# Optimization experiments

Hardware: AMD Instinct MI355X
Metric: run time of the kernel (lower is better)

The kernel has to match this reference:

```python
import jax, jax.numpy as jnp
import numpy as np

N_ITERS = 3   # Routing default n_iters
EPS = 1e-5    # variance floor added to sig2
LN_EPS = 1e-5 # torch LayerNorm eps


def _routing(a_inp, mu_inp, W, Bias, beta_use, beta_ign):
    """Heinsen routing (gaussian p_model).
    a_inp: [b, n_i]; mu_inp: [b, n_i, c, d_inp]
    W: [1 or n_i, n_o, d_inp, d_out]; Bias: [n_o, c, d_out]; betas: [n_o].
    """
    if W.shape[0] == 1:  # weights shared across input capsules (n_inp not fixed)
        V = jnp.einsum('jdh,bicd->bijch', W[0], mu_inp) + Bias
    else:
        V = jnp.einsum('ijdh,bicd->bijch', W, mu_inp) + Bias
    n_out = V.shape[2]
    fa = jax.nn.sigmoid(a_inp)[..., None]          # [b, n_i, 1]
    R = jnp.full(V.shape[:3], 1.0 / n_out, dtype=V.dtype)
    a_out = mu_out = sig2 = Vm2 = None
    for it in range(N_ITERS):
        # E-step
        if it > 0:
            log_p = (-jnp.einsum('bijch,bjch->bij', Vm2, 1.0 / (2.0 * sig2))
                     - 0.5 * jnp.log(sig2).sum(axis=(-2, -1))[:, None, :])
            R = jax.nn.softmax(jax.nn.log_sigmoid(a_out)[:, None, :] + log_p, axis=-1)
        # D-step
        D_use = fa * R                              # [b, n_i, n_o]
        D_sum = D_use.sum(axis=-2)                  # [b, n_o]
        # M-step
        a_out = beta_use * D_sum - beta_ign * (fa.sum(axis=-2) - D_sum)
        nR = D_use / D_sum[:, None, :]
        mu_out = jnp.einsum('bij,bijch->bjch', nR, V)
        Vm2 = jnp.square(V - mu_out[:, None])
        sig2 = jnp.einsum('bij,bijch->bjch', nR, Vm2) + EPS
    return a_out, mu_out, sig2


def setup_inputs() -> dict:
    B, T = 32, 128
    d_depth, d_emb, d_cap, n_parts, n_classes = 13, 1024, 16, 64, 5
    key = jax.random.key(0)
    ks = jax.random.split(key, 8)
    mask = jax.random.uniform(ks[0], (B, T), jnp.float32, 0.05, 0.95)  # in (0,1) so logit is finite
    embs = jax.random.normal(ks[1], (B, T, d_depth, d_emb), jnp.float32)
    depth_emb = jax.random.normal(ks[2], (d_depth, d_emb), jnp.float32) * 0.02
    ln_w = jnp.ones((d_emb,), jnp.float32)
    ln_b = jnp.zeros((d_emb,), jnp.float32)
    dp_w = jax.random.normal(ks[3], (n_parts, d_emb), jnp.float32) * np.sqrt(2.0 / d_emb)  # kaiming
    dp_b = jnp.zeros((n_parts,), jnp.float32)
    # Routing 1: d_cov=1, d_inp=n_parts, d_out=d_cap, n_out=n_parts, n_inp shared (-1)
    W1 = jax.random.normal(ks[4], (1, n_parts, n_parts, d_cap), jnp.float32) / n_parts
    B1 = jnp.zeros((n_parts, 1, d_cap), jnp.float32)
    bu1 = jnp.zeros((n_parts,), jnp.float32)
    bi1 = jnp.zeros((n_parts,), jnp.float32)
    # Routing 2: d_cov=1, d_inp=d_cap, d_out=d_cap, n_out=n_classes, n_inp=n_parts
    W2 = jax.random.normal(ks[5], (n_parts, n_classes, d_cap, d_cap), jnp.float32) / d_cap
    B2 = jnp.zeros((n_classes, 1, d_cap), jnp.float32)
    bu2 = jnp.zeros((n_classes,), jnp.float32)
    bi2 = jnp.zeros((n_classes,), jnp.float32)
    return dict(mask=mask, embs=embs, depth_emb=depth_emb, ln_w=ln_w, ln_b=ln_b,
                dp_w=dp_w, dp_b=dp_b, W1=W1, B1=B1, bu1=bu1, bi1=bi1,
                W2=W2, B2=B2, bu2=bu2, bi2=bi2)


def reference(mask, embs, depth_emb, ln_w, ln_b, dp_w, dp_b,
              W1, B1, bu1, bi1, W2, B2, bu2, bi2):
    B = mask.shape[0]
    d_depth = embs.shape[-2]
    # input activations: logit(mask), repeated over depth
    a = jnp.log(mask / (1.0 - mask))                       # [B, T]
    a = jnp.broadcast_to(a[..., None], a.shape + (d_depth,)).reshape(B, -1)  # [B, T*d_depth]
    # detect_parts: LayerNorm -> Linear -> Swish
    x = embs + depth_emb
    m = x.mean(axis=-1, keepdims=True)
    v = ((x - m) ** 2).mean(axis=-1, keepdims=True)        # biased var (torch LayerNorm)
    xn = (x - m) * jax.lax.rsqrt(v + LN_EPS) * ln_w + ln_b
    h = jnp.einsum('btde,pe->btdp', xn, dp_w) + dp_b
    mu = h * jax.nn.sigmoid(h)                             # Swish
    mu = mu.reshape(B, -1, 1, mu.shape[-1])                # [B, T*d_depth, 1, n_parts]
    a, mu, sig2 = _routing(a, mu, W1, B1, bu1, bi1)
    a, mu, sig2 = _routing(a, mu, W2, B2, bu2, bi2)
    return a, mu, sig2
```

## Files before the change

kernel.cpp:

```cpp
#include <hip/hip_runtime.h>
#include <hip/hip_bf16.h>

constexpr int BQ = 32;
constexpr int TT = 128;
constexpr int DD = 13;
constexpr int E  = 1024;
constexpr int P  = 64;
constexpr int C  = 16;
constexpr int NC = 5;
constexpr int NI = TT * DD;
constexpr int NROWS = BQ * NI;
constexpr int S1 = 1092;

__global__ void k_sumfa(const float* __restrict__ mask, float* __restrict__ sumfa)
{
    const int b = blockIdx.x, tid = threadIdx.x;
    float v = mask[b * TT + tid];
#pragma unroll
    for (int off = 32; off > 0; off >>= 1) v += __shfl_xor(v, off);
    __shared__ float p2[2];
    if ((tid & 63) == 0) p2[tid >> 6] = v;
    __syncthreads();
    if (tid == 0) sumfa[b] = (float)DD * (p2[0] + p2[1]);
}

__global__ void k0_pre(const float* __restrict__ ln_w, const float* __restrict__ ln_b,
                       const float* __restrict__ dp_w, const float* __restrict__ dp_b,
                       const float* __restrict__ W1,
                       float* __restrict__ c1t, float* __restrict__ c2t,
                       float* __restrict__ W1m)
{
    const int blk = blockIdx.x, tid = threadIdx.x;
    if (blk < 64) {
        float a0 = 0.f, a1 = 0.f;
        for (int k = tid; k < E; k += 256) {
            const float wv = dp_w[(size_t)blk * E + k];
            a0 = fmaf(ln_w[k], wv, a0);
            a1 = fmaf(ln_b[k], wv, a1);
        }
#pragma unroll
        for (int off = 32; off > 0; off >>= 1) {
            a0 += __shfl_xor(a0, off);
            a1 += __shfl_xor(a1, off);
        }
        __shared__ float r2[2][4];
        if ((tid & 63) == 0) { r2[0][tid >> 6] = a0; r2[1][tid >> 6] = a1; }
        __syncthreads();
        if (tid == 0) {
            c1t[blk] = r2[0][0] + r2[0][1] + r2[0][2] + r2[0][3];
            c2t[blk] = r2[1][0] + r2[1][1] + r2[1][2] + r2[1][3] + dp_b[blk];
        }
    } else {
        const int t = (blk - 64) * 256 + tid;
        const int d = t >> 10, col = t & 1023;
        W1m[t] = W1[((size_t)(col >> 4) * 64 + d) * 16 + (col & 15)];
    }
}

__global__ __launch_bounds__(256, 2) void
k1a(const float* __restrict__ embs, const float* __restrict__ depth_emb,
    const float* __restrict__ ln_w, const float* __restrict__ dp_w,
    const float* __restrict__ c1t, const float* __restrict__ c2t,
    float* __restrict__ V)
{
    __shared__ float xs[16 * S1];
    __shared__ float rmean[16], rrstd[16];
    float* hpar = xs;
    const int tid = threadIdx.x;
    const int c4 = tid & 15, q = tid >> 4;
    const int wv = tid >> 6;
    const int row0 = blockIdx.x * 64;

    for (int rt = 0; rt < 4; ++rt) {
        const int r0g = row0 + rt * 16;
        {
            const int sr = tid >> 4;
            const int sk = (tid & 15) * 4;
            const int grow = r0g + sr;
            const float* xr = embs + (size_t)grow * E;
            const float* dr = depth_emb + (size_t)(grow % DD) * E;
            float s = 0.f, s2 = 0.f;
#pragma unroll
            for (int m = 0; m < 16; ++m) {
                const int k = sk + m * 64;
                float4 a = *reinterpret_cast<const float4*>(xr + k);
                const float4 dd = *reinterpret_cast<const float4*>(dr + k);
                a.x += dd.x; a.y += dd.y; a.z += dd.z; a.w += dd.w;
                *reinterpret_cast<float4*>(xs + sr * S1 + sk + m * 68) = a;
                s += a.x + a.y + a.z + a.w;
                s2 = fmaf(a.x, a.x, fmaf(a.y, a.y, fmaf(a.z, a.z, fmaf(a.w, a.w, s2))));
            }
#pragma unroll
            for (int off = 8; off > 0; off >>= 1) {
                s += __shfl_xor(s, off);
                s2 += __shfl_xor(s2, off);
            }
            if ((tid & 15) == 0) {
                const float mean = s * (1.f / E);
                const float var = s2 * (1.f / E) - mean * mean;
                rmean[sr] = mean;
                rrstd[sr] = rsqrtf(var + 1e-5f);
            }
        }
        __syncthreads();
        float acc[16][4];
#pragma unroll
        for (int r = 0; r < 16; ++r)
#pragma unroll
            for (int cc = 0; cc < 4; ++cc) acc[r][cc] = 0.f;

        for (int sub = 0; sub < 4; ++sub) {
            const int kb = q * 64 + sub * 16;
            float4 wr_[4][4];
            {
                float4 lw[4];
#pragma unroll
                for (int f = 0; f < 4; ++f)
                    lw[f] = *reinterpret_cast<const float4*>(ln_w + kb + f * 4);
#pragma unroll
                for (int cc = 0; cc < 4; ++cc) {
                    const float* wp = dp_w + (size_t)(c4 * 4 + cc) * E + kb;
#pragma unroll
                    for (int f = 0; f < 4; ++f) {
                        float4 t = *reinterpret_cast<const float4*>(wp + f * 4);
                        t.x *= lw[f].x; t.y *= lw[f].y; t.z *= lw[f].z; t.w *= lw[f].w;
                        wr_[cc][f] = t;
                    }
                }
            }
            const int xbase = q * 68 + sub * 16;
#pragma unroll
            for (int r = 0; r < 16; ++r) {
#pragma unroll
                for (int f = 0; f < 4; ++f) {
                    const float4 x4 = *reinterpret_cast<const float4*>(xs + r * S1 + xbase + f * 4);
#pragma unroll
                    for (int cc = 0; cc < 4; ++cc) {
                        acc[r][cc] = fmaf(x4.x, wr_[cc][f].x, acc[r][cc]);
                        acc[r][cc] = fmaf(x4.y, wr_[cc][f].y, acc[r][cc]);
                        acc[r][cc] = fmaf(x4.z, wr_[cc][f].z, acc[r][cc]);
                        acc[r][cc] = fmaf(x4.w, wr_[cc][f].w, acc[r][cc]);
                    }
                }
            }
        }
#pragma unroll
        for (int r = 0; r < 16; ++r)
#pragma unroll
            for (int cc = 0; cc < 4; ++cc) {
                float v = acc[r][cc];
                v += __shfl_xor(v, 16);
                v += __shfl_xor(v, 32);
                acc[r][cc] = v;
            }
        __syncthreads();
        if ((tid & 48) == 0) {
#pragma unroll
            for (int r = 0; r < 16; ++r)
                *reinterpret_cast<float4*>(hpar + ((wv * 16 + r) * 68 + c4 * 4)) =
                    make_float4(acc[r][0], acc[r][1], acc[r][2], acc[r][3]);
        }
        __syncthreads();
        {
            const int er = tid >> 4, ec = tid & 15;
            float4 sum = make_float4(0.f, 0.f, 0.f, 0.f);
#pragma unroll
            for (int w = 0; w < 4; ++w) {
                const float4 hp = *reinterpret_cast<const float4*>(hpar + ((w * 16 + er) * 68 + ec * 4));
                sum.x += hp.x; sum.y += hp.y; sum.z += hp.z; sum.w += hp.w;
            }
            const float mean = rmean[er], rstd = rrstd[er];
            const float4 cv1 = *reinterpret_cast<const float4*>(c1t + ec * 4);
            const float4 cv2 = *reinterpret_cast<const float4*>(c2t + ec * 4);
            float4 h, mu;
            h.x = fmaf(rstd, sum.x - mean * cv1.x, cv2.x);
            h.y = fmaf(rstd, sum.y - mean * cv1.y, cv2.y);
            h.z = fmaf(rstd, sum.z - mean * cv1.z, cv2.z);
            h.w = fmaf(rstd, sum.w - mean * cv1.w, cv2.w);
            mu.x = h.x / (1.f + __expf(-h.x));
            mu.y = h.y / (1.f + __expf(-h.y));
            mu.z = h.z / (1.f + __expf(-h.z));
            mu.w = h.w / (1.f + __expf(-h.w));
            *reinterpret_cast<float4*>(V + (size_t)(r0g + er) * 1024 + 960 + ec * 4) = mu;
        }
        __syncthreads();
    }
}

__global__ __launch_bounds__(256) void
k1b(const float* __restrict__ W1m, const float* __restrict__ B1, float* __restrict__ V)
{
    __shared__ float muL[16][64];
    const int tid = threadIdx.x;
    const int row0 = blockIdx.x * 16;
#pragma unroll
    for (int q = 0; q < 4; ++q) {
        const int idx = q * 256 + tid;
        muL[idx >> 6][idx & 63] = V[(size_t)(row0 + (idx >> 6)) * 1024 + 960 + (idx & 63)];
    }
    __syncthreads();
    const int c4 = tid;
    float4 acc[16];
    const float4 bv = *reinterpret_cast<const float4*>(B1 + c4 * 4);
#pragma unroll
    for (int r = 0; r < 16; ++r) acc[r] = bv;

    for (int kc = 0; kc < 64; kc += 8) {
        float4 wreg[8];
#pragma unroll
        for (int kk = 0; kk < 8; ++kk)
            wreg[kk] = *reinterpret_cast<const float4*>(W1m + (size_t)(kc + kk) * 1024 + c4 * 4);
#pragma unroll
        for (int r = 0; r < 16; ++r) {
            const float4 ma = *reinterpret_cast<const float4*>(&muL[r][kc]);
            const float4 mb = *reinterpret_cast<const float4*>(&muL[r][kc + 4]);
            float4 a = acc[r];
            a.x = fmaf(ma.x, wreg[0].x, a.x); a.y = fmaf(ma.x, wreg[0].y, a.y);
            a.z = fmaf(ma.x, wreg[0].z, a.z); a.w = fmaf(ma.x, wreg[0].w, a.w);
            a.x = fmaf(ma.y, wreg[1].x, a.x); a.y = fmaf(ma.y, wreg[1].y, a.y);
            a.z = fmaf(ma.y, wreg[1].z, a.z); a.w = fmaf(ma.y, wreg[1].w, a.w);
            a.x = fmaf(ma.z, wreg[2].x, a.x); a.y = fmaf(ma.z, wreg[2].y, a.y);
            a.z = fmaf(ma.z, wreg[2].z, a.z); a.w = fmaf(ma.z, wreg[2].w, a.w);
            a.x = fmaf(ma.w, wreg[3].x, a.x); a.y = fmaf(ma.w, wreg[3].y, a.y);
            a.z = fmaf(ma.w, wreg[3].z, a.z); a.w = fmaf(ma.w, wreg[3].w, a.w);
            a.x = fmaf(mb.x, wreg[4].x, a.x); a.y = fmaf(mb.x, wreg[4].y, a.y);
            a.z = fmaf(mb.x, wreg[4].z, a.z); a.w = fmaf(mb.x, wreg[4].w, a.w);
            a.x = fmaf(mb.y, wreg[5].x, a.x); a.y = fmaf(mb.y, wreg[5].y, a.y);
            a.z = fmaf(mb.y, wreg[5].z, a.z); a.w = fmaf(mb.y, wreg[5].w, a.w);
            a.x = fmaf(mb.z, wreg[6].x, a.x); a.y = fmaf(mb.z, wreg[6].y, a.y);
            a.z = fmaf(mb.z, wreg[6].z, a.z); a.w = fmaf(mb.z, wreg[6].w, a.w);
            a.x = fmaf(mb.w, wreg[7].x, a.x); a.y = fmaf(mb.w, wreg[7].y, a.y);
            a.z = fmaf(mb.w, wreg[7].z, a.z); a.w = fmaf(mb.w, wreg[7].w, a.w);
            acc[r] = a;
        }
    }
#pragma unroll
    for (int r = 0; r < 16; ++r)
        *reinterpret_cast<float4*>(V + (size_t)(row0 + r) * 1024 + c4 * 4) = acc[r];
}

__global__ __launch_bounds__(256) void
kG(const float* __restrict__ V, const float* __restrict__ mask,
   float* __restrict__ G, float* __restrict__ F)
{
    __shared__ float mus[64][65];
    __shared__ float faL[64];
    const int tid = threadIdx.x;
    const int b = blockIdx.x / 26, ch = blockIdx.x % 26;
    const int i0 = ch * 64;
#pragma unroll
    for (int s = 0; s < 16; ++s) {
        const int idx = s * 256 + tid;
        mus[idx >> 6][idx & 63] =
            V[(size_t)(b * NI + i0 + (idx >> 6)) * 1024 + 960 + (idx & 63)];
    }
    if (tid < 64) faL[tid] = mask[b * TT + (i0 + tid) / DD];
    __syncthreads();
    const int a0 = tid & 15, b0 = tid >> 4;
    float g[4][4];
    float f4[4] = {0.f, 0.f, 0.f, 0.f};
#pragma unroll
    for (int aa = 0; aa < 4; ++aa)
#pragma unroll
        for (int bb = 0; bb < 4; ++bb) g[aa][bb] = 0.f;
    for (int i = 0; i < 64; ++i) {
        const float fa = faL[i];
        float va[4], vb[4];
#pragma unroll
        for (int s = 0; s < 4; ++s) {
            va[s] = fa * mus[i][a0 + s * 16];
            vb[s] = mus[i][b0 + s * 16];
        }
#pragma unroll
        for (int aa = 0; aa < 4; ++aa)
#pragma unroll
            for (int bb = 0; bb < 4; ++bb) g[aa][bb] = fmaf(va[aa], vb[bb], g[aa][bb]);
        if (b0 == 0) {
#pragma unroll
            for (int aa = 0; aa < 4; ++aa) f4[aa] += va[aa];
        }
    }
#pragma unroll
    for (int aa = 0; aa < 4; ++aa)
#pragma unroll
        for (int bb = 0; bb < 4; ++bb)
            atomicAdd(&G[((size_t)b << 12) + (size_t)(a0 + aa * 16) * 64 + (b0 + bb * 16)],
                      g[aa][bb]);
    if (b0 == 0) {
#pragma unroll
        for (int aa = 0; aa < 4; ++aa) atomicAdd(&F[b * 64 + aa * 16 + a0], f4[aa]);
    }
}

__global__ __launch_bounds__(256) void
kGf(const float* __restrict__ G, const float* __restrict__ F,
    const float* __restrict__ sumfa, const float* __restrict__ W1m,
    const float* __restrict__ B1, float* __restrict__ Smu,
    float* __restrict__ SV2, float* __restrict__ Dsum)
{
    __shared__ float Gm[64][65];
    __shared__ float Fm[64];
    const int b = blockIdx.x >> 2, p = blockIdx.x & 3;
    const int tid = threadIdx.x;
#pragma unroll
    for (int s = 0; s < 16; ++s) {
        const int idx = s * 256 + tid;
        Gm[idx >> 6][idx & 63] = G[((size_t)b << 12) + idx];
    }
    if (tid < 64) Fm[tid] = F[b * 64 + tid];
    __syncthreads();
    const int col = p * 256 + tid;
    float w[64];
#pragma unroll
    for (int d = 0; d < 64; ++d) w[d] = W1m[d * 1024 + col];
    float fw = 0.f;
#pragma unroll
    for (int d = 0; d < 64; ++d) fw = fmaf(Fm[d], w[d], fw);
    float quad = 0.f;
#pragma unroll
    for (int d1 = 0; d1 < 64; ++d1) {
        float t1 = 0.f;
#pragma unroll
        for (int d2 = 0; d2 < 64; ++d2) t1 = fmaf(Gm[d1][d2], w[d2], t1);
        quad = fmaf(w[d1], t1, quad);
    }
    const float sf = sumfa[b];
    const float b1 = B1[col];
    Smu[((size_t)b << 10) + col] = (fw + sf * b1) * (1.f / 64.f);
    SV2[((size_t)b << 10) + col] = (quad + 2.f * b1 * fw + sf * b1 * b1) * (1.f / 64.f);
    if (p == 0 && tid < 64) Dsum[b * 64 + tid] = sf * (1.f / 64.f);
}

__global__ __launch_bounds__(256) void
k2_pass(const float* __restrict__ V, const float* __restrict__ mask,
        const float* __restrict__ c1v, const float* __restrict__ ivv,
        const float* __restrict__ c0v, float* __restrict__ Smu,
        float* __restrict__ SV2, float* __restrict__ Dsum, const int it)
{
    __shared__ float lacc[P][34];
    const int tid = threadIdx.x, wave = tid >> 6, j = tid & 63;
    const int b = blockIdx.x / (NI / 64);
    const int tile = blockIdx.x % (NI / 64);
    for (int k = tid; k < P * 34; k += 256) (&lacc[0][0])[k] = 0.f;

    float4 C1a, C1b, C1c, C1d, IVa, IVb, IVc, IVd;
    float c0 = 0.f;
    C1a = C1b = C1c = C1d = IVa = IVb = IVc = IVd = make_float4(0.f, 0.f, 0.f, 0.f);
    if (it > 0) {
        const float4* cp = reinterpret_cast<const float4*>(c1v + ((size_t)b * P + j) * C);
        const float4* ip = reinterpret_cast<const float4*>(ivv + ((size_t)b * P + j) * C);
        C1a = cp[0]; C1b = cp[1]; C1c = cp[2]; C1d = cp[3];
        IVa = ip[0]; IVb = ip[1]; IVc = ip[2]; IVd = ip[3];
        c0 = c0v[(size_t)b * P + j];
    }
    const int i0 = tile * 64 + wave * 16;
    const float* vb = V + ((size_t)(b * NI) + i0) * 1024 + (j << 4);
    const float* mrow = mask + b * TT;

    float4 SMa, SMb, SMc, SMd, Qa, Qb, Qc, Qd;
    SMa = SMb = SMc = SMd = Qa = Qb = Qc = Qd = make_float4(0.f, 0.f, 0.f, 0.f);
    float dsum = 0.f;
    __syncthreads();

    auto proc = [&](const float4 va, const float4 vB, const float4 vc, const float4 vd, const int i) {
        float w;
        const float fam = mrow[i / DD];
        if (it > 0) {
            float q = c0;
            q = fmaf(va.x, fmaf(-va.x, IVa.x, C1a.x), q);
            q = fmaf(va.y, fmaf(-va.y, IVa.y, C1a.y), q);
            q = fmaf(va.z, fmaf(-va.z, IVa.z, C1a.z), q);
            q = fmaf(va.w, fmaf(-va.w, IVa.w, C1a.w), q);
            q = fmaf(vB.x, fmaf(-vB.x, IVb.x, C1b.x), q);
            q = fmaf(vB.y, fmaf(-vB.y, IVb.y, C1b.y), q);
            q = fmaf(vB.z, fmaf(-vB.z, IVb.z, C1b.z), q);
            q = fmaf(vB.w, fmaf(-vB.w, IVb.w, C1b.w), q);
            q = fmaf(vc.x, fmaf(-vc.x, IVc.x, C1c.x), q);
            q = fmaf(vc.y, fmaf(-vc.y, IVc.y, C1c.y), q);
            q = fmaf(vc.z, fmaf(-vc.z, IVc.z, C1c.z), q);
            q = fmaf(vc.w, fmaf(-vc.w, IVc.w, C1c.w), q);
            q = fmaf(vd.x, fmaf(-vd.x, IVd.x, C1d.x), q);
            q = fmaf(vd.y, fmaf(-vd.y, IVd.y, C1d.y), q);
            q = fmaf(vd.z, fmaf(-vd.z, IVd.z, C1d.z), q);
            q = fmaf(vd.w, fmaf(-vd.w, IVd.w, C1d.w), q);
            float m = q;
            m = fmaxf(m, __shfl_xor(m, 32));
            m = fmaxf(m, __shfl_xor(m, 16));
            m = fmaxf(m, __shfl_xor(m, 8));
            m = fmaxf(m, __shfl_xor(m, 4));
            m = fmaxf(m, __shfl_xor(m, 2));
            m = fmaxf(m, __shfl_xor(m, 1));
            const float e = __expf(q - m);
            float ss = e;
            ss += __shfl_xor(ss, 32);
            ss += __shfl_xor(ss, 16);
            ss += __shfl_xor(ss, 8);
            ss += __shfl_xor(ss, 4);
            ss += __shfl_xor(ss, 2);
            ss += __shfl_xor(ss, 1);
            w = fam * (e / ss);
        } else {
            w = fam * (1.f / 64.f);
        }
        dsum += w;
        SMa.x = fmaf(w, va.x, SMa.x); Qa.x = fmaf(w * va.x, va.x, Qa.x);
        SMa.y = fmaf(w, va.y, SMa.y); Qa.y = fmaf(w * va.y, va.y, Qa.y);
        SMa.z = fmaf(w, va.z, SMa.z); Qa.z = fmaf(w * va.z, va.z, Qa.z);
        SMa.w = fmaf(w, va.w, SMa.w); Qa.w = fmaf(w * va.w, va.w, Qa.w);
        SMb.x = fmaf(w, vB.x, SMb.x); Qb.x = fmaf(w * vB.x, vB.x, Qb.x);
        SMb.y = fmaf(w, vB.y, SMb.y); Qb.y = fmaf(w * vB.y, vB.y, Qb.y);
        SMb.z = fmaf(w, vB.z, SMb.z); Qb.z = fmaf(w * vB.z, vB.z, Qb.z);
        SMb.w = fmaf(w, vB.w, SMb.w); Qb.w = fmaf(w * vB.w, vB.w, Qb.w);
        SMc.x = fmaf(w, vc.x, SMc.x); Qc.x = fmaf(w * vc.x, vc.x, Qc.x);
        SMc.y = fmaf(w, vc.y, SMc.y); Qc.y = fmaf(w * vc.y, vc.y, Qc.y);
        SMc.z = fmaf(w, vc.z, SMc.z); Qc.z = fmaf(w * vc.z, vc.z, Qc.z);
        SMc.w = fmaf(w, vc.w, SMc.w); Qc.w = fmaf(w * vc.w, vc.w, Qc.w);
        SMd.x = fmaf(w, vd.x, SMd.x); Qd.x = fmaf(w * vd.x, vd.x, Qd.x);
        SMd.y = fmaf(w, vd.y, SMd.y); Qd.y = fmaf(w * vd.y, vd.y, Qd.y);
        SMd.z = fmaf(w, vd.z, SMd.z); Qd.z = fmaf(w * vd.z, vd.z, Qd.z);
        SMd.w = fmaf(w, vd.w, SMd.w); Qd.w = fmaf(w * vd.w, vd.w, Qd.w);
    };

    float4 A0, A1, A2, A3, B0, B1r, B2, B3;
    {
        const float4* p = reinterpret_cast<const float4*>(vb);
        A0 = p[0]; A1 = p[1]; A2 = p[2]; A3 = p[3];
    }
#pragma unroll
    for (int ss = 0; ss < 16; ss += 2) {
        {
            const float4* p = reinterpret_cast<const float4*>(vb + (size_t)(ss + 1) * 1024);
            B0 = p[0]; B1r = p[1]; B2 = p[2]; B3 = p[3];
        }
        proc(A0, A1, A2, A3, i0 + ss);
        if (ss + 2 < 16) {
            const float4* p = reinterpret_cast<const float4*>(vb + (size_t)(ss + 2) * 1024);
            A0 = p[0]; A1 = p[1]; A2 = p[2]; A3 = p[3];
        }
        proc(B0, B1r, B2, B3, i0 + ss + 1);
    }

    atomicAdd(&lacc[j][0],  SMa.x); atomicAdd(&lacc[j][1],  SMa.y);
    atomicAdd(&lacc[j][2],  SMa.z); atomicAdd(&lacc[j][3],  SMa.w);
    atomicAdd(&lacc[j][4],  SMb.x); atomicAdd(&lacc[j][5],  SMb.y);
    atomicAdd(&lacc[j][6],  SMb.z); atomicAdd(&lacc[j][7],  SMb.w);
    atomicAdd(&lacc[j][8],  SMc.x); atomicAdd(&lacc[j][9],  SMc.y);
    atomicAdd(&lacc[j][10], SMc.z); atomicAdd(&lacc[j][11], SMc.w);
    atomicAdd(&lacc[j][12], SMd.x); atomicAdd(&lacc[j][13], SMd.y);
    atomicAdd(&lacc[j][14], SMd.z); atomicAdd(&lacc[j][15], SMd.w);
    atomicAdd(&lacc[j][16], Qa.x);  atomicAdd(&lacc[j][17], Qa.y);
    atomicAdd(&lacc[j][18], Qa.z);  atomicAdd(&lacc[j][19], Qa.w);
    atomicAdd(&lacc[j][20], Qb.x);  atomicAdd(&lacc[j][21], Qb.y);
    atomicAdd(&lacc[j][22], Qb.z);  atomicAdd(&lacc[j][23], Qb.w);
    atomicAdd(&lacc[j][24], Qc.x);  atomicAdd(&lacc[j][25], Qc.y);
    atomicAdd(&lacc[j][26], Qc.z);  atomicAdd(&lacc[j][27], Qc.w);
    atomicAdd(&lacc[j][28], Qd.x);  atomicAdd(&lacc[j][29], Qd.y);
    atomicAdd(&lacc[j][30], Qd.z);  atomicAdd(&lacc[j][31], Qd.w);
    atomicAdd(&lacc[j][32], dsum);
    __syncthreads();

    for (int k = tid; k < P * 33; k += 256) {
        const int jj = k / 33, r = k % 33;
        const float v = lacc[jj][r];
        if (r < 16)      atomicAdd(&Smu[((size_t)b * P + jj) * C + r], v);
        else if (r < 32) atomicAdd(&SV2[((size_t)b * P + jj) * C + (r - 16)], v);
        else             atomicAdd(&Dsum[(size_t)b * P + jj], v);
    }
}

__global__ void k2f(float* __restrict__ Smu, float* __restrict__ SV2,
                    float* __restrict__ Dsum, const float* __restrict__ sumfa,
                    const float* __restrict__ bu, const float* __restrict__ bi,
                    float* __restrict__ muo, float* __restrict__ ivv,
                    float* __restrict__ c1v, float* __restrict__ c0v,
                    float* __restrict__ a1)
{
    const int t = blockIdx.x * blockDim.x + threadIdx.x;
    if (t >= BQ * P) return;
    const int b = t / P, j = t % P;
    const float ds = Dsum[t];
    const float inv = 1.f / ds;
    const float ao = bu[j] * ds - bi[j] * (sumfa[b] - ds);
    a1[t] = ao;
    const float lsg = (ao < 0.f) ? (ao - log1pf(__expf(ao))) : (-log1pf(__expf(-ao)));
    float sumlog = 0.f, moiv = 0.f;
#pragma unroll
    for (int h = 0; h < C; ++h) {
        const float m = Smu[t * C + h] * inv;
        const float s2 = fmaxf(SV2[t * C + h] * inv - m * m, 0.f) + 1e-5f;
        const float iv = 0.5f / s2;
        muo[t * C + h] = m;
        ivv[t * C + h] = iv;
        c1v[t * C + h] = 2.f * m * iv;
        sumlog += logf(s2);
        moiv += m * m * iv;
        Smu[t * C + h] = 0.f;
        SV2[t * C + h] = 0.f;
    }
    Dsum[t] = 0.f;
    c0v[t] = lsg - 0.5f * sumlog - moiv;
}

__global__ void k3_routing2(const float* __restrict__ muo, const float* __restrict__ a1,
                            const float* __restrict__ W2, const float* __restrict__ B2,
                            const float* __restrict__ bu2, const float* __restrict__ bi2,
                            float* __restrict__ out)
{
    __shared__ float mu1L[P][C];
    __shared__ float faL[P];
    __shared__ float V2L[P][NC][C];
    __shared__ float RL[P][NC];
    __shared__ float mu2L[NC][C];
    __shared__ float s2L[NC][C];
    __shared__ float isL[NC][C];
    __shared__ float dsL[NC];
    __shared__ float biasL[NC];
    __shared__ float a2L[NC];
    __shared__ float sumfa2s;
    const int b = blockIdx.x, tid = threadIdx.x;

    for (int k = tid; k < P * C; k += 256) (&mu1L[0][0])[k] = muo[(size_t)b * P * C + k];
    if (tid < P) {
        const float a = a1[(size_t)b * P + tid];
        faL[tid] = 1.f / (1.f + __expf(-a));
    }
    __syncthreads();
    if (tid == 0) {
        float s = 0.f;
        for (int i = 0; i < P; ++i) s += faL[i];
        sumfa2s = s;
    }
    {
        const int i = tid >> 2, hq = tid & 3;
        for (int jj = 0; jj < NC; ++jj) {
            float4 acc = *reinterpret_cast<const float4*>(B2 + jj * C + hq * 4);
            const float* wp = W2 + ((size_t)(i * NC + jj) * C) * C + hq * 4;
#pragma unroll
            for (int d = 0; d < C; ++d) {
                const float m = mu1L[i][d];
                const float4 w4 = *reinterpret_cast<const float4*>(wp + d * C);
                acc.x += m * w4.x; acc.y += m * w4.y; acc.z += m * w4.z; acc.w += m * w4.w;
            }
            *reinterpret_cast<float4*>(&V2L[i][jj][hq * 4]) = acc;
        }
    }
    __syncthreads();

    for (int it = 0; it < 3; ++it) {
        if (tid < P) {
            const int i = tid;
            if (it == 0) {
#pragma unroll
                for (int jj = 0; jj < NC; ++jj) RL[i][jj] = 1.f / NC;
            } else {
                float sc[NC];
                float m = -3.4e38f;
#pragma unroll
                for (int jj = 0; jj < NC; ++jj) {
                    float q = 0.f;
#pragma unroll
                    for (int h = 0; h < C; ++h) {
                        const float d = V2L[i][jj][h] - mu2L[jj][h];
                        q += d * d * isL[jj][h];
                    }
                    sc[jj] = biasL[jj] - q;
                    m = fmaxf(m, sc[jj]);
                }
                float sum = 0.f;
#pragma unroll
                for (int jj = 0; jj < NC; ++jj) { sc[jj] = __expf(sc[jj] - m); sum += sc[jj]; }
                const float invs = 1.f / sum;
#pragma unroll
                for (int jj = 0; jj < NC; ++jj) RL[i][jj] = sc[jj] * invs;
            }
        }
        __syncthreads();
        if (tid < NC) {
            float ds = 0.f;
            for (int i = 0; i < P; ++i) ds += faL[i] * RL[i][tid];
            dsL[tid] = ds;
        }
        __syncthreads();
        if (tid < NC * C) {
            const int jj = tid / C, h = tid % C;
            float smu = 0.f, sv2 = 0.f;
            for (int i = 0; i < P; ++i) {
                const float w = faL[i] * RL[i][jj];
                const float v = V2L[i][jj][h];
                smu += w * v;
                sv2 += w * v * v;
            }
            const float inv = 1.f / dsL[jj];
            const float m = smu * inv;
            const float s2 = fmaxf(sv2 * inv - m * m, 0.f) + 1e-5f;
            mu2L[jj][h] = m;
            s2L[jj][h] = s2;
            isL[jj][h] = 0.5f / s2;
        }
        __syncthreads();
        if (tid < NC) {
            const float ds = dsL[tid];
            const float ao = bu2[tid] * ds - bi2[tid] * (sumfa2s - ds);
            a2L[tid] = ao;
            const float lsg = (ao < 0.f) ? (ao - log1pf(__expf(ao))) : (-log1pf(__expf(-ao)));
            float sl = 0.f;
#pragma unroll
            for (int h = 0; h < C; ++h) sl += logf(s2L[tid][h]);
            biasL[tid] = lsg - 0.5f * sl;
        }
        __syncthreads();
    }

    if (tid < NC) out[(size_t)b * NC + tid] = a2L[tid];
    if (tid < NC * C) {
        const int jj = tid / C, h = tid % C;
        out[BQ * NC + ((size_t)b * NC + jj) * C + h] = mu2L[jj][h];
        out[BQ * NC + BQ * NC * C + ((size_t)b * NC + jj) * C + h] = s2L[jj][h];
    }
}

extern "C" void kernel_launch(void* const* d_in, const int* in_sizes, int n_in,
                              void* d_out, int out_size, void* d_ws, size_t ws_size,
                              hipStream_t stream)
{
    (void)in_sizes; (void)n_in; (void)out_size; (void)ws_size;
    const float* mask      = (const float*)d_in[0];
    const float* embs      = (const float*)d_in[1];
    const float* depth_emb = (const float*)d_in[2];
    const float* ln_w      = (const float*)d_in[3];
    const float* ln_b      = (const float*)d_in[4];
    const float* dp_w      = (const float*)d_in[5];
    const float* dp_b      = (const float*)d_in[6];
    const float* W1        = (const float*)d_in[7];
    const float* B1        = (const float*)d_in[8];
    const float* bu1       = (const float*)d_in[9];
    const float* bi1       = (const float*)d_in[10];
    const float* W2        = (const float*)d_in[11];
    const float* B2        = (const float*)d_in[12];
    const float* bu2       = (const float*)d_in[13];
    const float* bi2       = (const float*)d_in[14];
    float* out = (float*)d_out;

    float* ws = (float*)d_ws;
    size_t o = 0;
    float* V     = ws + o; o += (size_t)NROWS * 1024;
    float* c1t   = ws + o; o += 64;
    float* c2t   = ws + o; o += 64;
    float* W1m   = ws + o; o += 65536;
    float* G     = ws + o; o += (size_t)BQ * 64 * 64;
    float* F     = ws + o; o += (size_t)BQ * 64;
    float* Smu   = ws + o; o += (size_t)BQ * P * C;
    float* SV2   = ws + o; o += (size_t)BQ * P * C;
    float* Dsum  = ws + o; o += (size_t)BQ * P;
    float* muo   = ws + o; o += (size_t)BQ * P * C;
    float* ivv   = ws + o; o += (size_t)BQ * P * C;
    float* c1v   = ws + o; o += (size_t)BQ * P * C;
    float* c0v   = ws + o; o += (size_t)BQ * P;
    float* a1    = ws + o; o += (size_t)BQ * P;
    float* sumfa = ws + o; o += BQ;

    k0_pre<<<320, 256, 0, stream>>>(ln_w, ln_b, dp_w, dp_b, W1, c1t, c2t, W1m);
    k_sumfa<<<BQ, 128, 0, stream>>>(mask, sumfa);
    hipMemsetAsync(G, 0, (size_t)(BQ * 64 * 64 + BQ * 64) * sizeof(float), stream);
    k1a<<<NROWS / 64, 256, 0, stream>>>(embs, depth_emb, ln_w, dp_w, c1t, c2t, V);
    kG<<<BQ * 26, 256, 0, stream>>>(V, mask, G, F);
    k1b<<<NROWS / 16, 256, 0, stream>>>(W1m, B1, V);
    kGf<<<BQ * 4, 256, 0, stream>>>(G, F, sumfa, W1m, B1, Smu, SV2, Dsum);
    k2f<<<(BQ * P) / 256, 256, 0, stream>>>(Smu, SV2, Dsum, sumfa, bu1, bi1,
                                            muo, ivv, c1v, c0v, a1);
    for (int it = 1; it < 3; ++it) {
        k2_pass<<<BQ * (NI / 64), 256, 0, stream>>>(V, mask, c1v, ivv, c0v,
                                                    Smu, SV2, Dsum, it);
        k2f<<<(BQ * P) / 256, 256, 0, stream>>>(Smu, SV2, Dsum, sumfa, bu1, bi1,
                                                muo, ivv, c1v, c0v, a1);
    }
    k3_routing2<<<BQ, 256, 0, stream>>>(muo, a1, W2, B2, bu2, bi2, out);
}
```

Baseline: 1.085 ms.

## Restructure part-detection GEMM per row and interleave V capsule layout

```diff
diff --git a/kernel.cpp b/kernel.cpp
--- a/kernel.cpp
+++ b/kernel.cpp
@@ -10,7 +10,7 @@
 constexpr int NC = 5;
 constexpr int NI = TT * DD;
 constexpr int NROWS = BQ * NI;
-constexpr int S1 = 1092;
+
 
 __global__ void k_sumfa(const float* __restrict__ mask, float* __restrict__ sumfa)
 {
@@ -26,9 +26,10 @@
 
 __global__ void k0_pre(const float* __restrict__ ln_w, const float* __restrict__ ln_b,
                        const float* __restrict__ dp_w, const float* __restrict__ dp_b,
-                       const float* __restrict__ W1,
+                       const float* __restrict__ W1, const float* __restrict__ B1,
                        float* __restrict__ c1t, float* __restrict__ c2t,
-                       float* __restrict__ W1m)
+                       float* __restrict__ W1m, float* __restrict__ W1mP,
+                       float* __restrict__ gwP, float* __restrict__ B1P)
 {
     const int blk = blockIdx.x, tid = threadIdx.x;
     if (blk < 64) {
@@ -50,193 +51,131 @@
             c1t[blk] = r2[0][0] + r2[0][1] + r2[0][2] + r2[0][3];
             c2t[blk] = r2[1][0] + r2[1][1] + r2[1][2] + r2[1][3] + dp_b[blk];
         }
-    } else {
+    } else if (blk < 320) {
         const int t = (blk - 64) * 256 + tid;
         const int d = t >> 10, col = t & 1023;
         W1m[t] = W1[((size_t)(col >> 4) * 64 + d) * 16 + (col & 15)];
-    }
-}
-
-__global__ __launch_bounds__(256, 2) void
+    } else if (blk < 576) {
+        const int t = (blk - 320) * 256 + tid;
+        const int d = t >> 10, pcol = t & 1023;
+        const int hq = pcol >> 8, j = (pcol >> 2) & 63, m = pcol & 3;
+        W1mP[t] = W1[((size_t)j * 64 + d) * 16 + hq * 4 + m];
+    } else if (blk < 832) {
+        const int t = (blk - 576) * 256 + tid;
+        const int kq = t >> 8, rem = t & 255, p = rem >> 2, tt = rem & 3;
+        const int k = kq * 4 + tt;
+        gwP[t] = ln_w[k] * dp_w[(size_t)p * E + k];
+    } else {
+        const int t = (blk - 832) * 256 + tid;
+        const int hq = t >> 8, j = (t >> 2) & 63, m = t & 3;
+        B1P[t] = B1[j * 16 + hq * 4 + m];
+    }
+}
+
+__global__ __launch_bounds__(256) void
 k1a(const float* __restrict__ embs, const float* __restrict__ depth_emb,
-    const float* __restrict__ ln_w, const float* __restrict__ dp_w,
-    const float* __restrict__ c1t, const float* __restrict__ c2t,
-    float* __restrict__ V)
-{
-    __shared__ float xs[16 * S1];
-    __shared__ float rmean[16], rrstd[16];
-    float* hpar = xs;
+    const float* __restrict__ gwP, const float* __restrict__ c1t,
+    const float* __restrict__ c2t, float* __restrict__ V)
+{
+    __shared__ float hs[64][65];
     const int tid = threadIdx.x;
-    const int c4 = tid & 15, q = tid >> 4;
-    const int wv = tid >> 6;
+    const int lane = tid & 63;
+    const int cg = __builtin_amdgcn_readfirstlane(tid >> 6);
     const int row0 = blockIdx.x * 64;
-
-    for (int rt = 0; rt < 4; ++rt) {
-        const int r0g = row0 + rt * 16;
-        {
-            const int sr = tid >> 4;
-            const int sk = (tid & 15) * 4;
-            const int grow = r0g + sr;
-            const float* xr = embs + (size_t)grow * E;
-            const float* dr = depth_emb + (size_t)(grow % DD) * E;
-            float s = 0.f, s2 = 0.f;
-#pragma unroll
-            for (int m = 0; m < 16; ++m) {
-                const int k = sk + m * 64;
-                float4 a = *reinterpret_cast<const float4*>(xr + k);
-                const float4 dd = *reinterpret_cast<const float4*>(dr + k);
-                a.x += dd.x; a.y += dd.y; a.z += dd.z; a.w += dd.w;
-                *reinterpret_cast<float4*>(xs + sr * S1 + sk + m * 68) = a;
-                s += a.x + a.y + a.z + a.w;
-                s2 = fmaf(a.x, a.x, fmaf(a.y, a.y, fmaf(a.z, a.z, fmaf(a.w, a.w, s2))));
-            }
-#pragma unroll
-            for (int off = 8; off > 0; off >>= 1) {
-                s += __shfl_xor(s, off);
-                s2 += __shfl_xor(s2, off);
-            }
-            if ((tid & 15) == 0) {
-                const float mean = s * (1.f / E);
-                const float var = s2 * (1.f / E) - mean * mean;
-                rmean[sr] = mean;
-                rrstd[sr] = rsqrtf(var + 1e-5f);
-            }
-        }
-        __syncthreads();
-        float acc[16][4];
-#pragma unroll
-        for (int r = 0; r < 16; ++r)
-#pragma unroll
-            for (int cc = 0; cc < 4; ++cc) acc[r][cc] = 0.f;
-
-        for (int sub = 0; sub < 4; ++sub) {
-            const int kb = q * 64 + sub * 16;
-            float4 wr_[4][4];
-            {
-                float4 lw[4];
-#pragma unroll
-                for (int f = 0; f < 4; ++f)
-                    lw[f] = *reinterpret_cast<const float4*>(ln_w + kb + f * 4);
-#pragma unroll
-                for (int cc = 0; cc < 4; ++cc) {
-                    const float* wp = dp_w + (size_t)(c4 * 4 + cc) * E + kb;
-#pragma unroll
-                    for (int f = 0; f < 4; ++f) {
-                        float4 t = *reinterpret_cast<const float4*>(wp + f * 4);
-                        t.x *= lw[f].x; t.y *= lw[f].y; t.z *= lw[f].z; t.w *= lw[f].w;
-                        wr_[cc][f] = t;
-                    }
-                }
-            }
-            const int xbase = q * 68 + sub * 16;
-#pragma unroll
-            for (int r = 0; r < 16; ++r) {
-#pragma unroll
-                for (int f = 0; f < 4; ++f) {
-                    const float4 x4 = *reinterpret_cast<const float4*>(xs + r * S1 + xbase + f * 4);
-#pragma unroll
-                    for (int cc = 0; cc < 4; ++cc) {
-                        acc[r][cc] = fmaf(x4.x, wr_[cc][f].x, acc[r][cc]);
-                        acc[r][cc] = fmaf(x4.y, wr_[cc][f].y, acc[r][cc]);
-                        acc[r][cc] = fmaf(x4.z, wr_[cc][f].z, acc[r][cc]);
-                        acc[r][cc] = fmaf(x4.w, wr_[cc][f].w, acc[r][cc]);
-                    }
-                }
-            }
-        }
-#pragma unroll
-        for (int r = 0; r < 16; ++r)
-#pragma unroll
-            for (int cc = 0; cc < 4; ++cc) {
-                float v = acc[r][cc];
-                v += __shfl_xor(v, 16);
-                v += __shfl_xor(v, 32);
-                acc[r][cc] = v;
-            }
-        __syncthreads();
-        if ((tid & 48) == 0) {
-#pragma unroll
-            for (int r = 0; r < 16; ++r)
-                *reinterpret_cast<float4*>(hpar + ((wv * 16 + r) * 68 + c4 * 4)) =
-                    make_float4(acc[r][0], acc[r][1], acc[r][2], acc[r][3]);
-        }
-        __syncthreads();
-        {
-            const int er = tid >> 4, ec = tid & 15;
-            float4 sum = make_float4(0.f, 0.f, 0.f, 0.f);
-#pragma unroll
-            for (int w = 0; w < 4; ++w) {
-                const float4 hp = *reinterpret_cast<const float4*>(hpar + ((w * 16 + er) * 68 + ec * 4));
-                sum.x += hp.x; sum.y += hp.y; sum.z += hp.z; sum.w += hp.w;
-            }
-            const float mean = rmean[er], rstd = rrstd[er];
-            const float4 cv1 = *reinterpret_cast<const float4*>(c1t + ec * 4);
-            const float4 cv2 = *reinterpret_cast<const float4*>(c2t + ec * 4);
-            float4 h, mu;
-            h.x = fmaf(rstd, sum.x - mean * cv1.x, cv2.x);
-            h.y = fmaf(rstd, sum.y - mean * cv1.y, cv2.y);
-            h.z = fmaf(rstd, sum.z - mean * cv1.z, cv2.z);
-            h.w = fmaf(rstd, sum.w - mean * cv1.w, cv2.w);
-            mu.x = h.x / (1.f + __expf(-h.x));
-            mu.y = h.y / (1.f + __expf(-h.y));
-            mu.z = h.z / (1.f + __expf(-h.z));
-            mu.w = h.w / (1.f + __expf(-h.w));
-            *reinterpret_cast<float4*>(V + (size_t)(r0g + er) * 1024 + 960 + ec * 4) = mu;
-        }
-        __syncthreads();
+    const int row = row0 + lane;
+    const float* xr = embs + (size_t)row * E;
+    const float* dr = depth_emb + (size_t)(row % DD) * E;
+
+    float acc[16];
+#pragma unroll
+    for (int c = 0; c < 16; ++c) acc[c] = 0.f;
+    float s = 0.f, s2 = 0.f;
+
+#pragma unroll 4
+    for (int kq = 0; kq < 256; ++kq) {
+        float4 x4 = *reinterpret_cast<const float4*>(xr + kq * 4);
+        const float4 d4 = *reinterpret_cast<const float4*>(dr + kq * 4);
+        x4.x += d4.x; x4.y += d4.y; x4.z += d4.z; x4.w += d4.w;
+        s += x4.x + x4.y + x4.z + x4.w;
+        s2 = fmaf(x4.x, x4.x, fmaf(x4.y, x4.y, fmaf(x4.z, x4.z, fmaf(x4.w, x4.w, s2))));
+        const float4* wq = reinterpret_cast<const float4*>(gwP + ((size_t)kq << 8) + (cg << 6));
+#pragma unroll
+        for (int c = 0; c < 16; ++c) {
+            const float4 w = wq[c];
+            acc[c] = fmaf(x4.x, w.x, acc[c]);
+            acc[c] = fmaf(x4.y, w.y, acc[c]);
+            acc[c] = fmaf(x4.z, w.z, acc[c]);
+            acc[c] = fmaf(x4.w, w.w, acc[c]);
+        }
+    }
+    const float mean = s * (1.f / E);
+    const float var  = s2 * (1.f / E) - mean * mean;
+    const float rstd = rsqrtf(var + 1e-5f);
+#pragma unroll
+    for (int c = 0; c < 16; ++c) {
+        const int p = cg * 16 + c;
+        const float h = fmaf(rstd, acc[c] - mean * c1t[p], c2t[p]);
+        hs[lane][p] = h / (1.f + __expf(-h));
+    }
+    __syncthreads();
+    {
+        const int rr = tid >> 2, seg = tid & 3;
+        float* dst = V + (size_t)(row0 + rr) * 1024 + 960 + seg * 16;
+#pragma unroll
+        for (int m = 0; m < 4; ++m) {
+            float4 o;
+            o.x = hs[rr][seg * 16 + m * 4 + 0];
+            o.y = hs[rr][seg * 16 + m * 4 + 1];
+            o.z = hs[rr][seg * 16 + m * 4 + 2];
+            o.w = hs[rr][seg * 16 + m * 4 + 3];
+            *reinterpret_cast<float4*>(dst + m * 4) = o;
+        }
     }
 }
 
 __global__ __launch_bounds__(256) void
-k1b(const float* __restrict__ W1m, const float* __restrict__ B1, float* __restrict__ V)
-{
-    __shared__ float muL[16][64];
-    const int tid = threadIdx.x;
+k1b(const float* __restrict__ W1mP, const float* __restrict__ B1P, float* __restrict__ V)
+{
+    const int c4 = threadIdx.x;
     const int row0 = blockIdx.x * 16;
-#pragma unroll
-    for (int q = 0; q < 4; ++q) {
-        const int idx = q * 256 + tid;
-        muL[idx >> 6][idx & 63] = V[(size_t)(row0 + (idx >> 6)) * 1024 + 960 + (idx & 63)];
-    }
-    __syncthreads();
-    const int c4 = tid;
     float4 acc[16];
-    const float4 bv = *reinterpret_cast<const float4*>(B1 + c4 * 4);
+    const float4 bv = *reinterpret_cast<const float4*>(B1P + (c4 << 2));
 #pragma unroll
     for (int r = 0; r < 16; ++r) acc[r] = bv;
 
-    for (int kc = 0; kc < 64; kc += 8) {
-        float4 wreg[8];
-#pragma unroll
-        for (int kk = 0; kk < 8; ++kk)
-            wreg[kk] = *reinterpret_cast<const float4*>(W1m + (size_t)(kc + kk) * 1024 + c4 * 4);
+#pragma unroll 2
+    for (int kq = 0; kq < 16; ++kq) {
+        float4 wreg[4];
+#pragma unroll
+        for (int t = 0; t < 4; ++t)
+            wreg[t] = *reinterpret_cast<const float4*>(
+                W1mP + (size_t)(kq * 4 + t) * 1024 + (c4 << 2));
 #pragma unroll
         for (int r = 0; r < 16; ++r) {
-            const float4 ma = *reinterpret_cast<const float4*>(&muL[r][kc]);
-            const float4 mb = *reinterpret_cast<const float4*>(&muL[r][kc + 4]);
-            float4 a = acc[r];
-            a.x = fmaf(ma.x, wreg[0].x, a.x); a.y = fmaf(ma.x, wreg[0].y, a.y);
-            a.z = fmaf(ma.x, wreg[0].z, a.z); a.w = fmaf(ma.x, wreg[0].w, a.w);
-            a.x = fmaf(ma.y, wreg[1].x, a.x); a.y = fmaf(ma.y, wreg[1].y, a.y);
-            a.z = fmaf(ma.y, wreg[1].z, a.z); a.w = fmaf(ma.y, wreg[1].w, a.w);
-            a.x = fmaf(ma.z, wreg[2].x, a.x); a.y = fmaf(ma.z, wreg[2].y, a.y);
-            a.z = fmaf(ma.z, wreg[2].z, a.z); a.w = fmaf(ma.z, wreg[2].w, a.w);
-            a.x = fmaf(ma.w, wreg[3].x, a.x); a.y = fmaf(ma.w, wreg[3].y, a.y);
-            a.z = fmaf(ma.w, wreg[3].z, a.z); a.w = fmaf(ma.w, wreg[3].w, a.w);
-            a.x = fmaf(mb.x, wreg[4].x, a.x); a.y = fmaf(mb.x, wreg[4].y, a.y);
-            a.z = fmaf(mb.x, wreg[4].z, a.z); a.w = fmaf(mb.x, wreg[4].w, a.w);
-            a.x = fmaf(mb.y, wreg[5].x, a.x); a.y = fmaf(mb.y, wreg[5].y, a.y);
-            a.z = fmaf(mb.y, wreg[5].z, a.z); a.w = fmaf(mb.y, wreg[5].w, a.w);
-            a.x = fmaf(mb.z, wreg[6].x, a.x); a.y = fmaf(mb.z, wreg[6].y, a.y);
-            a.z = fmaf(mb.z, wreg[6].z, a.z); a.w = fmaf(mb.z, wreg[6].w, a.w);
-            a.x = fmaf(mb.w, wreg[7].x, a.x); a.y = fmaf(mb.w, wreg[7].y, a.y);
-            a.z = fmaf(mb.w, wreg[7].z, a.z); a.w = fmaf(mb.w, wreg[7].w, a.w);
-            acc[r] = a;
-        }
-    }
+            const float4 sm = *reinterpret_cast<const float4*>(
+                V + (size_t)(row0 + r) * 1024 + 960 + kq * 4);
+            acc[r].x = fmaf(sm.x, wreg[0].x, acc[r].x);
+            acc[r].y = fmaf(sm.x, wreg[0].y, acc[r].y);
+            acc[r].z = fmaf(sm.x, wreg[0].z, acc[r].z);
+            acc[r].w = fmaf(sm.x, wreg[0].w, acc[r].w);
+            acc[r].x = fmaf(sm.y, wreg[1].x, acc[r].x);
+            acc[r].y = fmaf(sm.y, wreg[1].y, acc[r].y);
+            acc[r].z = fmaf(sm.y, wreg[1].z, acc[r].z);
+            acc[r].w = fmaf(sm.y, wreg[1].w, acc[r].w);
+            acc[r].x = fmaf(sm.z, wreg[2].x, acc[r].x);
+            acc[r].y = fmaf(sm.z, wreg[2].y, acc[r].y);
+            acc[r].z = fmaf(sm.z, wreg[2].z, acc[r].z);
+            acc[r].w = fmaf(sm.z, wreg[2].w, acc[r].w);
+            acc[r].x = fmaf(sm.w, wreg[3].x, acc[r].x);
+            acc[r].y = fmaf(sm.w, wreg[3].y, acc[r].y);
+            acc[r].z = fmaf(sm.w, wreg[3].z, acc[r].z);
+            acc[r].w = fmaf(sm.w, wreg[3].w, acc[r].w);
+        }
+    }
+    __syncthreads();
 #pragma unroll
     for (int r = 0; r < 16; ++r)
-        *reinterpret_cast<float4*>(V + (size_t)(row0 + r) * 1024 + c4 * 4) = acc[r];
+        *reinterpret_cast<float4*>(V + (size_t)(row0 + r) * 1024 + (c4 << 2)) = acc[r];
 }
 
 __global__ __launch_bounds__(256) void
@@ -354,7 +293,7 @@
         c0 = c0v[(size_t)b * P + j];
     }
     const int i0 = tile * 64 + wave * 16;
-    const float* vb = V + ((size_t)(b * NI) + i0) * 1024 + (j << 4);
+    const float* vb = V + ((size_t)(b * NI) + i0) * 1024 + (j << 2);
     const float* mrow = mask + b * TT;
 
     float4 SMa, SMb, SMc, SMd, Qa, Qb, Qc, Qd;
@@ -423,19 +362,27 @@
 
     float4 A0, A1, A2, A3, B0, B1r, B2, B3;
     {
-        const float4* p = reinterpret_cast<const float4*>(vb);
-        A0 = p[0]; A1 = p[1]; A2 = p[2]; A3 = p[3];
+        A0 = *reinterpret_cast<const float4*>(vb + 0);
+        A1 = *reinterpret_cast<const float4*>(vb + 256);
+        A2 = *reinterpret_cast<const float4*>(vb + 512);
+        A3 = *reinterpret_cast<const float4*>(vb + 768);
     }
 #pragma unroll
     for (int ss = 0; ss < 16; ss += 2) {
         {
-            const float4* p = reinterpret_cast<const float4*>(vb + (size_t)(ss + 1) * 1024);
-            B0 = p[0]; B1r = p[1]; B2 = p[2]; B3 = p[3];
+            const float* p = vb + (size_t)(ss + 1) * 1024;
+            B0 = *reinterpret_cast<const float4*>(p + 0);
+            B1r = *reinterpret_cast<const float4*>(p + 256);
+            B2 = *reinterpret_cast<const float4*>(p + 512);
+            B3 = *reinterpret_cast<const float4*>(p + 768);
         }
         proc(A0, A1, A2, A3, i0 + ss);
         if (ss + 2 < 16) {
-            const float4* p = reinterpret_cast<const float4*>(vb + (size_t)(ss + 2) * 1024);
-            A0 = p[0]; A1 = p[1]; A2 = p[2]; A3 = p[3];
+            const float* p = vb + (size_t)(ss + 2) * 1024;
+            A0 = *reinterpret_cast<const float4*>(p + 0);
+            A1 = *reinterpret_cast<const float4*>(p + 256);
+            A2 = *reinterpret_cast<const float4*>(p + 512);
+            A3 = *reinterpret_cast<const float4*>(p + 768);
         }
         proc(B0, B1r, B2, B3, i0 + ss + 1);
     }
@@ -647,6 +594,9 @@
     float* c1t   = ws + o; o += 64;
     float* c2t   = ws + o; o += 64;
     float* W1m   = ws + o; o += 65536;
+    float* W1mP  = ws + o; o += 65536;
+    float* gwP   = ws + o; o += 65536;
+    float* B1P   = ws + o; o += 1024;
     float* G     = ws + o; o += (size_t)BQ * 64 * 64;
     float* F     = ws + o; o += (size_t)BQ * 64;
     float* Smu   = ws + o; o += (size_t)BQ * P * C;
@@ -659,12 +609,13 @@
     float* a1    = ws + o; o += (size_t)BQ * P;
     float* sumfa = ws + o; o += BQ;
 
-    k0_pre<<<320, 256, 0, stream>>>(ln_w, ln_b, dp_w, dp_b, W1, c1t, c2t, W1m);
+    k0_pre<<<836, 256, 0, stream>>>(ln_w, ln_b, dp_w, dp_b, W1, B1,
+                                    c1t, c2t, W1m, W1mP, gwP, B1P);
     k_sumfa<<<BQ, 128, 0, stream>>>(mask, sumfa);
     hipMemsetAsync(G, 0, (size_t)(BQ * 64 * 64 + BQ * 64) * sizeof(float), stream);
-    k1a<<<NROWS / 64, 256, 0, stream>>>(embs, depth_emb, ln_w, dp_w, c1t, c2t, V);
+    k1a<<<NROWS / 64, 256, 0, stream>>>(embs, depth_emb, gwP, c1t, c2t, V);
     kG<<<BQ * 26, 256, 0, stream>>>(V, mask, G, F);
-    k1b<<<NROWS / 16, 256, 0, stream>>>(W1m, B1, V);
+    k1b<<<NROWS / 16, 256, 0, stream>>>(W1mP, B1P, V);
     kGf<<<BQ * 4, 256, 0, stream>>>(G, F, sumfa, W1m, B1, Smu, SV2, Dsum);
     k2f<<<(BQ * P) / 256, 256, 0, stream>>>(Smu, SV2, Dsum, sumfa, bu1, bi1,
                                             muo, ivv, c1v, c0v, a1);
```

Result: faster. 935.9 us (-13.7%).
